# Performance work log

Hardware: AMD Instinct MI355X
Metric: run time of the kernel (lower is better)

Reference implementation:

```python
import jax, jax.numpy as jnp
import numpy as np

B, IN_LEN, L = 32, 10, 16384
N_POLY, M_MODES, K_STR, CH, NB = 12, 6, 2, 20, 4


def _legendre_filters():
    # Midpoints of n equal intervals on [-1, 1]
    j = np.arange(N_POLY)
    xs = -1.0 + (2.0 * j + 1.0) / N_POLY
    fr = np.stack([np.polynomial.legendre.Legendre.basis(i)(xs) for i in range(M_MODES)])
    fd = fr * ((2.0 * np.arange(M_MODES) + 1.0) / N_POLY)[:, None]  # decomposition quadrature weights
    return fd[:, None, :].astype(np.float32), fr[:, None, :].astype(np.float32)


def _conv1d(x, w, stride=1):
    return jax.lax.conv_general_dilated(x, w, (stride,), 'VALID',
                                        dimension_numbers=('NCH', 'OIH', 'NCH'))


def setup_inputs() -> dict:
    key = jax.random.key(0)
    ks = jax.random.split(key, 7)
    sc = 0.1
    fd, fr = _legendre_filters()
    return {
        'input':   jax.random.normal(ks[0], (B, IN_LEN, L), jnp.float32),
        'w_first': jax.random.normal(ks[1], (CH, IN_LEN, 3), jnp.float32) * sc,
        'conv_a':  jax.random.normal(ks[2], (NB, CH, CH, 3), jnp.float32) * sc,
        'conv_b':  jax.random.normal(ks[3], (NB, CH, CH, 3), jnp.float32) * sc,
        'lin_m':   jax.random.normal(ks[4], (NB, CH, M_MODES, M_MODES), jnp.float32) * sc,
        'w11':     jax.random.normal(ks[5], (128, CH, 1), jnp.float32) * sc,
        'w_out':   jax.random.normal(ks[6], (1, 128, 1), jnp.float32) * sc,
        'filt_d':  jnp.asarray(fd),
        'filt_r':  jnp.asarray(fr),
    }


def reference(input, w_first, conv_a, conv_b, lin_m, w11, w_out, filt_d, filt_r):
    n, m, kk = N_POLY, M_MODES, K_STR
    s = n // kk                      # conv stride = 6
    nb = conv_a.shape[0]
    RR = (n // kk) * (kk - 1)        # 6
    recept = RR * nb + 1
    rc = 2
    gelu = lambda t: jax.nn.gelu(t, approximate=False)

    b, _, Lin = input.shape
    li = Lin + 2 * recept - 2
    half = n // 2
    r = half - li % half             # circular padding to make strided conv exact
    x = jnp.pad(input, ((0, 0), (0, 0), (recept, recept + r)), mode='wrap')
    x = _conv1d(x, w_first)          # (b, CH, l)
    c = x.shape[1]

    for i in range(nb):
        l = x.shape[-1]
        # local residual branch: conv3 -> gelu -> conv3
        linear_x = _conv1d(gelu(_conv1d(x, conv_a[i])), conv_b[i])  # (b, c, l-4)
        # Legendre decomposition: strided conv per (b,c) signal
        xr = x.reshape(b * c, 1, l)
        Lx = _conv1d(xr, filt_d / kk, stride=s)                     # (b*c, m, ll)
        ll = Lx.shape[-1]
        Lx = Lx.reshape(b, c, m, ll).transpose(0, 2, 1, 3).reshape(b, m * c, ll)
        # grouped 1x1 conv: groups=c consecutive chunks of size m over the (mode-major) channel axis
        Lg = Lx.reshape(b, c, m, ll)
        Lg = jnp.einsum('bgil,goi->bgol', Lg, lin_m[i])
        Lx2 = Lg.reshape(b, m * c, ll)
        Lx2 = Lx2.reshape(b, m, c, ll).transpose(0, 2, 1, 3).reshape(b * c, m, ll) * 2.0
        # conv_transpose1d (stride s, kernel n=2s) via overlap-add of two half-kernels
        y = jnp.einsum('xmt,mk->xtk', Lx2, (filt_r / kk)[:, 0, :])  # (b*c, ll, n)
        p1 = y[..., :s].reshape(b * c, ll * s)
        p2 = y[..., s:].reshape(b * c, ll * s)
        rec = jnp.pad(p1, ((0, 0), (0, s))) + jnp.pad(p2, ((0, 0), (s, 0)))  # (b*c, l)
        rec = rec.reshape(b, c, l)
        x = gelu(rec[:, :, RR:-RR] + linear_x[:, :, RR - rc:-(RR - rc)])

    x = gelu(jnp.einsum('bcl,oc->bol', x, w11[:, :, 0]))
    x = jnp.einsum('bcl,oc->bol', x, w_out[:, :, 0])
    return x[:, :, :-r]
```

## Files before the change

kernel.cpp:

```cpp
#include <hip/hip_runtime.h>
#include <math.h>

#define B_ 32
#define INLEN 10
#define LIN_ 16384
#define NPOLY 12
#define MM 6
#define CH 20
#define NB 4
#define RECEPT 25
#define L0 16434
#define TTILE 216
#define NW 37
#define XS_LEN 228
#define XS_PAD 229
#define GS_LEN 218
#define LXS_PAD 121
#define CCHUNK 5
#define COH 10

__device__ __forceinline__ float gelu_exact(float x) {
    return 0.5f * x * (1.0f + erff(x * 0.70710678118654752440f));
}

__global__ void k_first(const float* __restrict__ in, const float* __restrict__ wf,
                        float* __restrict__ out) {
    int t = blockIdx.x * blockDim.x + threadIdx.x;
    int b = blockIdx.y;
    if (t >= L0) return;
    const float* inb = in + (size_t)b * INLEN * LIN_;
    float xw[INLEN][3];
#pragma unroll
    for (int ci = 0; ci < INLEN; ++ci) {
#pragma unroll
        for (int k = 0; k < 3; ++k) {
            int idx = t + k - RECEPT;
            idx = (idx < 0) ? idx + LIN_ : (idx >= LIN_ ? idx - LIN_ : idx);
            xw[ci][k] = inb[ci * LIN_ + idx];
        }
    }
    float* outb = out + (size_t)b * CH * L0;
#pragma unroll
    for (int co = 0; co < CH; ++co) {
        float acc = 0.f;
#pragma unroll
        for (int ci = 0; ci < INLEN; ++ci)
#pragma unroll
            for (int k = 0; k < 3; ++k)
                acc = fmaf(xw[ci][k], wf[(co * INLEN + ci) * 3 + k], acc);
        outb[(size_t)co * L0 + t] = acc;
    }
}

__global__ __launch_bounds__(512, 2)
void k_block(const float* __restrict__ x, float* __restrict__ xn,
             const float* __restrict__ wA, const float* __restrict__ wB,
             const float* __restrict__ linm, const float* __restrict__ fd,
             const float* __restrict__ fr, int l) {
    const int lout = l - 12;
    const int tid  = threadIdx.x;
    const int t    = tid & 255;
    const int half = __builtin_amdgcn_readfirstlane(tid >> 8);
    const int cob  = half * COH;
    const int t0   = blockIdx.x * TTILE;
    const int b    = blockIdx.y;

    const float* wAh = wA + cob * CH * 3;
    const float* wBh = wB + cob * CH * 3;

    __shared__ float xs[CH][XS_PAD];
    __shared__ float lxs[NW][LXS_PAD];
    __shared__ float lm_s[CH * MM * MM];
    __shared__ float fr_s[MM * NPOLY];

    const float* xb = x + (size_t)b * CH * l;

    for (int i = tid; i < CH * MM * MM; i += 512) lm_s[i] = linm[i];
    for (int i = tid; i < MM * NPOLY; i += 512)   fr_s[i] = fr[i];

    for (int i = tid; i < CH * XS_LEN; i += 512) {
        int c = i / XS_LEN, p = i - c * XS_LEN;
        int gp = t0 + p;
        xs[c][p] = (gp < l) ? xb[(size_t)c * l + gp] : 0.f;
    }
    __syncthreads();

    for (int item = tid; item < NW * CH; item += 512) {
        int wl = item / CH, c = item - wl * CH;
        float xv[NPOLY];
#pragma unroll
        for (int k = 0; k < NPOLY; ++k) xv[k] = xs[c][6 * wl + k];
#pragma unroll
        for (int m = 0; m < MM; ++m) {
            float acc = 0.f;
#pragma unroll
            for (int k = 0; k < NPOLY; ++k)
                acc = fmaf(xv[k], fd[m * NPOLY + k], acc);
            lxs[wl][m * CH + c] = acc * 0.5f;
        }
    }

    float gv[COH];
    if (t < GS_LEN) {
#pragma unroll
        for (int co = 0; co < COH; ++co) gv[co] = 0.f;
#pragma unroll 1
        for (int cig = 0; cig < CH; cig += CCHUNK) {
            float xw[CCHUNK][3];
#pragma unroll
            for (int j = 0; j < CCHUNK; ++j) {
                xw[j][0] = xs[cig + j][t + 4];
                xw[j][1] = xs[cig + j][t + 5];
                xw[j][2] = xs[cig + j][t + 6];
            }
#pragma unroll
            for (int co = 0; co < COH; ++co) {
                float acc = gv[co];
#pragma unroll
                for (int j = 0; j < CCHUNK; ++j)
#pragma unroll
                    for (int k = 0; k < 3; ++k)
                        acc = fmaf(xw[j][k], wAh[(co * CH + cig + j) * 3 + k], acc);
                gv[co] = acc;
            }
        }
#pragma unroll
        for (int co = 0; co < COH; ++co) gv[co] = gelu_exact(gv[co]);
    }
    __syncthreads();

    if (t < GS_LEN) {
#pragma unroll
        for (int co = 0; co < COH; ++co) xs[cob + co][t] = gv[co];
    }

    for (int item = tid; item < NW * CH; item += 512) {
        int wl = item / CH, g = item - wl * CH;
        float iv[MM], ov[MM];
#pragma unroll
        for (int i = 0; i < MM; ++i) iv[i] = lxs[wl][g * MM + i];
#pragma unroll
        for (int o = 0; o < MM; ++o) {
            float acc = 0.f;
#pragma unroll
            for (int i = 0; i < MM; ++i)
                acc = fmaf(iv[i], lm_s[(g * MM + o) * MM + i], acc);
            ov[o] = acc;
        }
#pragma unroll
        for (int o = 0; o < MM; ++o) lxs[wl][g * MM + o] = ov[o];
    }
    __syncthreads();

    if (t < TTILE && t0 + t < lout) {
        const int tp = t;
        float acc[COH];
#pragma unroll
        for (int co = 0; co < COH; ++co) acc[co] = 0.f;
#pragma unroll 1
        for (int cig = 0; cig < CH; cig += CCHUNK) {
            float aw[CCHUNK][3];
#pragma unroll
            for (int j = 0; j < CCHUNK; ++j) {
                aw[j][0] = xs[cig + j][tp];
                aw[j][1] = xs[cig + j][tp + 1];
                aw[j][2] = xs[cig + j][tp + 2];
            }
#pragma unroll
            for (int co = 0; co < COH; ++co) {
                float a = acc[co];
#pragma unroll
                for (int j = 0; j < CCHUNK; ++j)
#pragma unroll
                    for (int k = 0; k < 3; ++k)
                        a = fmaf(aw[j][k], wBh[(co * CH + cig + j) * 3 + k], a);
                acc[co] = a;
            }
        }
        const int r1  = tp % 6;
        const int wl1 = tp / 6 + 1;
        float frA[MM], frB[MM];
#pragma unroll
        for (int m = 0; m < MM; ++m) {
            frA[m] = fr_s[m * NPOLY + r1];
            frB[m] = fr_s[m * NPOLY + r1 + 6];
        }
        float* xnb = xn + (size_t)b * CH * lout + (size_t)cob * lout;
#pragma unroll
        for (int co = 0; co < COH; ++co) {
            float rec = 0.f;
#pragma unroll
            for (int m = 0; m < MM; ++m) {
                rec = fmaf(lxs[wl1][m * CH + cob + co], frA[m], rec);
                rec = fmaf(lxs[wl1 - 1][m * CH + cob + co], frB[m], rec);
            }
            xnb[(size_t)co * lout + t0 + tp] = gelu_exact(acc[co] + rec);
        }
    }
}

__global__ void k_final(const float* __restrict__ x, const float* __restrict__ w11,
                        const float* __restrict__ wout, float* __restrict__ out) {
    int t = blockIdx.x * blockDim.x + threadIdx.x;
    int b = blockIdx.y;
    if (t >= LIN_) return;
    const int l4 = L0 - NB * 12;
    const float* xb = x + (size_t)b * CH * l4;
    float xv[CH];
#pragma unroll
    for (int c = 0; c < CH; ++c) xv[c] = xb[(size_t)c * l4 + t];
    float acc0 = 0.f, acc1 = 0.f, acc2 = 0.f, acc3 = 0.f;
    for (int h = 0; h < 128; h += 4) {
        float hv0 = 0.f, hv1 = 0.f, hv2 = 0.f, hv3 = 0.f;
#pragma unroll
        for (int c = 0; c < CH; ++c) {
            hv0 = fmaf(xv[c], w11[(h + 0) * CH + c], hv0);
            hv1 = fmaf(xv[c], w11[(h + 1) * CH + c], hv1);
            hv2 = fmaf(xv[c], w11[(h + 2) * CH + c], hv2);
            hv3 = fmaf(xv[c], w11[(h + 3) * CH + c], hv3);
        }
        acc0 = fmaf(gelu_exact(hv0), wout[h + 0], acc0);
        acc1 = fmaf(gelu_exact(hv1), wout[h + 1], acc1);
        acc2 = fmaf(gelu_exact(hv2), wout[h + 2], acc2);
        acc3 = fmaf(gelu_exact(hv3), wout[h + 3], acc3);
    }
    out[(size_t)b * LIN_ + t] = (acc0 + acc1) + (acc2 + acc3);
}

extern "C" void kernel_launch(void* const* d_in, const int* in_sizes, int n_in,
                              void* d_out, int out_size, void* d_ws, size_t ws_size,
                              hipStream_t stream) {
    const float* input   = (const float*)d_in[0];
    const float* w_first = (const float*)d_in[1];
    const float* conv_a  = (const float*)d_in[2];
    const float* conv_b  = (const float*)d_in[3];
    const float* lin_m   = (const float*)d_in[4];
    const float* w11     = (const float*)d_in[5];
    const float* w_out   = (const float*)d_in[6];
    const float* filt_d  = (const float*)d_in[7];
    const float* filt_r  = (const float*)d_in[8];
    float* out = (float*)d_out;

    const size_t bufElems = (size_t)B_ * CH * L0;
    float* xA = (float*)d_ws;
    float* xB = xA + bufElems;

    {
        dim3 grid((L0 + 255) / 256, B_);
        k_first<<<grid, 256, 0, stream>>>(input, w_first, xA);
    }

    int l = L0;
    float* cur = xA;
    float* nxt = xB;
    for (int i = 0; i < NB; ++i) {
        int lout  = l - 12;
        int tiles = (lout + TTILE - 1) / TTILE;
        dim3 grid(tiles, B_);
        k_block<<<grid, 512, 0, stream>>>(cur, nxt,
                                          conv_a + i * CH * CH * 3,
                                          conv_b + i * CH * CH * 3,
                                          lin_m + i * CH * MM * MM,
                                          filt_d, filt_r, l);
        float* tswap = cur; cur = nxt; nxt = tswap;
        l = lout;
    }

    {
        dim3 grid((LIN_ + 255) / 256, B_);
        k_final<<<grid, 256, 0, stream>>>(cur, w11, w_out, out);
    }
}
```

Before: 518.3 us.

## Fuse four residual block layers into one halo-tiled kernel using shared memory

```diff
diff --git a/kernel.cpp b/kernel.cpp
--- a/kernel.cpp
+++ b/kernel.cpp
@@ -11,13 +11,13 @@
 #define RECEPT 25
 #define L0 16434
 #define TTILE 216
-#define NW 37
-#define XS_LEN 228
-#define XS_PAD 229
-#define GS_LEN 218
+#define N0 264
+#define XP 265
+#define NWMAX 43
 #define LXS_PAD 121
 #define CCHUNK 5
 #define COH 10
+#define LOUT_F 16386
 
 __device__ __forceinline__ float gelu_exact(float x) {
     return 0.5f * x * (1.0f + erff(x * 0.70710678118654752440f));
@@ -53,148 +53,177 @@
 }
 
 __global__ __launch_bounds__(512, 2)
-void k_block(const float* __restrict__ x, float* __restrict__ xn,
-             const float* __restrict__ wA, const float* __restrict__ wB,
-             const float* __restrict__ linm, const float* __restrict__ fd,
-             const float* __restrict__ fr, int l) {
-    const int lout = l - 12;
+void k_fused(const float* __restrict__ x0, float* __restrict__ xout,
+             const float* __restrict__ conv_a, const float* __restrict__ conv_b,
+             const float* __restrict__ lin_m, const float* __restrict__ fd,
+             const float* __restrict__ fr) {
     const int tid  = threadIdx.x;
     const int t    = tid & 255;
     const int half = __builtin_amdgcn_readfirstlane(tid >> 8);
     const int cob  = half * COH;
-    const int t0   = blockIdx.x * TTILE;
+    const int G    = blockIdx.x * TTILE;
     const int b    = blockIdx.y;
 
-    const float* wAh = wA + cob * CH * 3;
-    const float* wBh = wB + cob * CH * 3;
-
-    __shared__ float xs[CH][XS_PAD];
-    __shared__ float lxs[NW][LXS_PAD];
+    __shared__ float xs[CH][XP];
+    __shared__ float lxs[NWMAX][LXS_PAD];
     __shared__ float lm_s[CH * MM * MM];
     __shared__ float fr_s[MM * NPOLY];
 
-    const float* xb = x + (size_t)b * CH * l;
-
-    for (int i = tid; i < CH * MM * MM; i += 512) lm_s[i] = linm[i];
-    for (int i = tid; i < MM * NPOLY; i += 512)   fr_s[i] = fr[i];
-
-    for (int i = tid; i < CH * XS_LEN; i += 512) {
-        int c = i / XS_LEN, p = i - c * XS_LEN;
-        int gp = t0 + p;
-        xs[c][p] = (gp < l) ? xb[(size_t)c * l + gp] : 0.f;
+    for (int i = tid; i < MM * NPOLY; i += 512) fr_s[i] = fr[i];
+
+    {
+        const float* xb = x0 + (size_t)b * CH * L0;
+        for (int i = tid; i < CH * N0; i += 512) {
+            int c = i / N0, p = i - c * N0;
+            int gp = G + p;
+            xs[c][p] = (gp < L0) ? xb[(size_t)c * L0 + gp] : 0.f;
+        }
     }
     __syncthreads();
 
-    for (int item = tid; item < NW * CH; item += 512) {
-        int wl = item / CH, c = item - wl * CH;
-        float xv[NPOLY];
-#pragma unroll
-        for (int k = 0; k < NPOLY; ++k) xv[k] = xs[c][6 * wl + k];
-#pragma unroll
-        for (int m = 0; m < MM; ++m) {
-            float acc = 0.f;
-#pragma unroll
-            for (int k = 0; k < NPOLY; ++k)
-                acc = fmaf(xv[k], fd[m * NPOLY + k], acc);
-            lxs[wl][m * CH + c] = acc * 0.5f;
-        }
-    }
-
-    float gv[COH];
-    if (t < GS_LEN) {
-#pragma unroll
-        for (int co = 0; co < COH; ++co) gv[co] = 0.f;
+    const float* wAi = conv_a;
+    const float* wBi = conv_b;
+    const float* lmi = lin_m;
+    int N = N0;
+
 #pragma unroll 1
-        for (int cig = 0; cig < CH; cig += CCHUNK) {
-            float xw[CCHUNK][3];
-#pragma unroll
-            for (int j = 0; j < CCHUNK; ++j) {
-                xw[j][0] = xs[cig + j][t + 4];
-                xw[j][1] = xs[cig + j][t + 5];
-                xw[j][2] = xs[cig + j][t + 6];
+    for (int layer = 0; layer < NB; ++layer) {
+        const int NW   = (N - 12) / 6 + 1;
+        const int GS   = N - 10;
+        const int NOUT = N - 12;
+
+        for (int item = tid; item < NW * CH; item += 512) {
+            int wl = item / CH, c = item - wl * CH;
+            float xv[NPOLY];
+#pragma unroll
+            for (int k = 0; k < NPOLY; ++k) xv[k] = xs[c][6 * wl + k];
+#pragma unroll
+            for (int m = 0; m < MM; ++m) {
+                float acc = 0.f;
+#pragma unroll
+                for (int k = 0; k < NPOLY; ++k)
+                    acc = fmaf(xv[k], fd[m * NPOLY + k], acc);
+                lxs[wl][m * CH + c] = acc * 0.5f;
+            }
+        }
+
+        for (int i = tid; i < CH * MM * MM; i += 512) lm_s[i] = lmi[i];
+
+        float gv[COH];
+        if (t < GS) {
+#pragma unroll
+            for (int co = 0; co < COH; ++co) gv[co] = 0.f;
+#pragma unroll 1
+            for (int cig = 0; cig < CH; cig += CCHUNK) {
+                float xw[CCHUNK][3];
+#pragma unroll
+                for (int j = 0; j < CCHUNK; ++j) {
+                    xw[j][0] = xs[cig + j][t + 4];
+                    xw[j][1] = xs[cig + j][t + 5];
+                    xw[j][2] = xs[cig + j][t + 6];
+                }
+#pragma unroll
+                for (int co = 0; co < COH; ++co) {
+                    float acc = gv[co];
+#pragma unroll
+                    for (int j = 0; j < CCHUNK; ++j)
+#pragma unroll
+                        for (int k = 0; k < 3; ++k)
+                            acc = fmaf(xw[j][k], wAi[((cob + co) * CH + cig + j) * 3 + k], acc);
+                    gv[co] = acc;
+                }
+            }
+#pragma unroll
+            for (int co = 0; co < COH; ++co) gv[co] = gelu_exact(gv[co]);
+        }
+        __syncthreads();
+
+        if (t < GS) {
+#pragma unroll
+            for (int co = 0; co < COH; ++co) xs[cob + co][t] = gv[co];
+        }
+
+        for (int item = tid; item < NW * CH; item += 512) {
+            int wl = item / CH, g = item - wl * CH;
+            float iv[MM], ov[MM];
+#pragma unroll
+            for (int i = 0; i < MM; ++i) iv[i] = lxs[wl][g * MM + i];
+#pragma unroll
+            for (int o = 0; o < MM; ++o) {
+                float acc = 0.f;
+#pragma unroll
+                for (int i = 0; i < MM; ++i)
+                    acc = fmaf(iv[i], lm_s[(g * MM + o) * MM + i], acc);
+                ov[o] = acc;
+            }
+#pragma unroll
+            for (int o = 0; o < MM; ++o) lxs[wl][g * MM + o] = ov[o];
+        }
+        __syncthreads();
+
+        float acc[COH];
+        const bool doD = (t < NOUT);
+        if (doD) {
+#pragma unroll
+            for (int co = 0; co < COH; ++co) acc[co] = 0.f;
+#pragma unroll 1
+            for (int cig = 0; cig < CH; cig += CCHUNK) {
+                float aw[CCHUNK][3];
+#pragma unroll
+                for (int j = 0; j < CCHUNK; ++j) {
+                    aw[j][0] = xs[cig + j][t];
+                    aw[j][1] = xs[cig + j][t + 1];
+                    aw[j][2] = xs[cig + j][t + 2];
+                }
+#pragma unroll
+                for (int co = 0; co < COH; ++co) {
+                    float a = acc[co];
+#pragma unroll
+                    for (int j = 0; j < CCHUNK; ++j)
+#pragma unroll
+                        for (int k = 0; k < 3; ++k)
+                            a = fmaf(aw[j][k], wBi[((cob + co) * CH + cig + j) * 3 + k], a);
+                    acc[co] = a;
+                }
+            }
+            const int r1  = t % 6;
+            const int wl1 = t / 6 + 1;
+            float frA[MM], frB[MM];
+#pragma unroll
+            for (int m = 0; m < MM; ++m) {
+                frA[m] = fr_s[m * NPOLY + r1];
+                frB[m] = fr_s[m * NPOLY + r1 + 6];
             }
 #pragma unroll
             for (int co = 0; co < COH; ++co) {
-                float acc = gv[co];
-#pragma unroll
-                for (int j = 0; j < CCHUNK; ++j)
-#pragma unroll
-                    for (int k = 0; k < 3; ++k)
-                        acc = fmaf(xw[j][k], wAh[(co * CH + cig + j) * 3 + k], acc);
-                gv[co] = acc;
-            }
-        }
-#pragma unroll
-        for (int co = 0; co < COH; ++co) gv[co] = gelu_exact(gv[co]);
-    }
-    __syncthreads();
-
-    if (t < GS_LEN) {
-#pragma unroll
-        for (int co = 0; co < COH; ++co) xs[cob + co][t] = gv[co];
-    }
-
-    for (int item = tid; item < NW * CH; item += 512) {
-        int wl = item / CH, g = item - wl * CH;
-        float iv[MM], ov[MM];
-#pragma unroll
-        for (int i = 0; i < MM; ++i) iv[i] = lxs[wl][g * MM + i];
-#pragma unroll
-        for (int o = 0; o < MM; ++o) {
-            float acc = 0.f;
-#pragma unroll
-            for (int i = 0; i < MM; ++i)
-                acc = fmaf(iv[i], lm_s[(g * MM + o) * MM + i], acc);
-            ov[o] = acc;
-        }
-#pragma unroll
-        for (int o = 0; o < MM; ++o) lxs[wl][g * MM + o] = ov[o];
-    }
-    __syncthreads();
-
-    if (t < TTILE && t0 + t < lout) {
-        const int tp = t;
-        float acc[COH];
-#pragma unroll
-        for (int co = 0; co < COH; ++co) acc[co] = 0.f;
-#pragma unroll 1
-        for (int cig = 0; cig < CH; cig += CCHUNK) {
-            float aw[CCHUNK][3];
-#pragma unroll
-            for (int j = 0; j < CCHUNK; ++j) {
-                aw[j][0] = xs[cig + j][tp];
-                aw[j][1] = xs[cig + j][tp + 1];
-                aw[j][2] = xs[cig + j][tp + 2];
-            }
-#pragma unroll
-            for (int co = 0; co < COH; ++co) {
-                float a = acc[co];
-#pragma unroll
-                for (int j = 0; j < CCHUNK; ++j)
-#pragma unroll
-                    for (int k = 0; k < 3; ++k)
-                        a = fmaf(aw[j][k], wBh[(co * CH + cig + j) * 3 + k], a);
-                acc[co] = a;
-            }
-        }
-        const int r1  = tp % 6;
-        const int wl1 = tp / 6 + 1;
-        float frA[MM], frB[MM];
-#pragma unroll
-        for (int m = 0; m < MM; ++m) {
-            frA[m] = fr_s[m * NPOLY + r1];
-            frB[m] = fr_s[m * NPOLY + r1 + 6];
-        }
-        float* xnb = xn + (size_t)b * CH * lout + (size_t)cob * lout;
-#pragma unroll
-        for (int co = 0; co < COH; ++co) {
-            float rec = 0.f;
-#pragma unroll
-            for (int m = 0; m < MM; ++m) {
-                rec = fmaf(lxs[wl1][m * CH + cob + co], frA[m], rec);
-                rec = fmaf(lxs[wl1 - 1][m * CH + cob + co], frB[m], rec);
-            }
-            xnb[(size_t)co * lout + t0 + tp] = gelu_exact(acc[co] + rec);
+                float rec = 0.f;
+#pragma unroll
+                for (int m = 0; m < MM; ++m) {
+                    rec = fmaf(lxs[wl1][m * CH + cob + co], frA[m], rec);
+                    rec = fmaf(lxs[wl1 - 1][m * CH + cob + co], frB[m], rec);
+                }
+                acc[co] = gelu_exact(acc[co] + rec);
+            }
+        }
+
+        if (layer < NB - 1) {
+            __syncthreads();
+            if (doD) {
+#pragma unroll
+                for (int co = 0; co < COH; ++co) xs[cob + co][t] = acc[co];
+            }
+            __syncthreads();
+            wAi += CH * CH * 3;
+            wBi += CH * CH * 3;
+            lmi += CH * MM * MM;
+            N -= 12;
+        } else {
+            if (doD && G + t < LOUT_F) {
+                float* xnb = xout + (size_t)b * CH * LOUT_F + (size_t)cob * LOUT_F;
+#pragma unroll
+                for (int co = 0; co < COH; ++co)
+                    xnb[(size_t)co * LOUT_F + G + t] = acc[co];
+            }
         }
     }
 }
@@ -204,11 +233,10 @@
     int t = blockIdx.x * blockDim.x + threadIdx.x;
     int b = blockIdx.y;
     if (t >= LIN_) return;
-    const int l4 = L0 - NB * 12;
-    const float* xb = x + (size_t)b * CH * l4;
+    const float* xb = x + (size_t)b * CH * LOUT_F;
     float xv[CH];
 #pragma unroll
-    for (int c = 0; c < CH; ++c) xv[c] = xb[(size_t)c * l4 + t];
+    for (int c = 0; c < CH; ++c) xv[c] = xb[(size_t)c * LOUT_F + t];
     float acc0 = 0.f, acc1 = 0.f, acc2 = 0.f, acc3 = 0.f;
     for (int h = 0; h < 128; h += 4) {
         float hv0 = 0.f, hv1 = 0.f, hv2 = 0.f, hv3 = 0.f;
@@ -249,25 +277,14 @@
         dim3 grid((L0 + 255) / 256, B_);
         k_first<<<grid, 256, 0, stream>>>(input, w_first, xA);
     }
-
-    int l = L0;
-    float* cur = xA;
-    float* nxt = xB;
-    for (int i = 0; i < NB; ++i) {
-        int lout  = l - 12;
-        int tiles = (lout + TTILE - 1) / TTILE;
+    {
+        int tiles = (LOUT_F + TTILE - 1) / TTILE;
         dim3 grid(tiles, B_);
-        k_block<<<grid, 512, 0, stream>>>(cur, nxt,
-                                          conv_a + i * CH * CH * 3,
-                                          conv_b + i * CH * CH * 3,
-                                          lin_m + i * CH * MM * MM,
-                                          filt_d, filt_r, l);
-        float* tswap = cur; cur = nxt; nxt = tswap;
-        l = lout;
-    }
-
+        k_fused<<<grid, 512, 0, stream>>>(xA, xB, conv_a, conv_b, lin_m,
+                                          filt_d, filt_r);
+    }
     {
         dim3 grid((LIN_ + 255) / 256, B_);
-        k_final<<<grid, 256, 0, stream>>>(cur, w11, w_out, out);
-    }
-}
+        k_final<<<grid, 256, 0, stream>>>(xB, w11, w_out, out);
+    }
+}
```

New measurement: 1.051 ms. 103% more time.
